# Kernel tuning notes

Measured on AMD Instinct MI355X. Metric: run time of the kernel, lower is better.

## Reference

```python
import jax, jax.numpy as jnp
import numpy as np

N, D = 65536, 1024  # points, in_dim == out_dim (required by the module's double use of linear.weight)


def setup_inputs() -> dict:
    key = jax.random.key(0)
    k_x, k_w, k_W, k_noise = jax.random.split(key, 4)
    x = jax.random.normal(k_x, (N, D), dtype=jnp.float32)
    w = jax.random.normal(k_w, (D,), dtype=jnp.float32)  # style vector (len == in_dim)
    # learned params of nn.Linear(in_dim, out_dim)
    W = jax.random.normal(k_W, (D, D), dtype=jnp.float32) * 0.02  # [out_dim, in_dim]
    b = jnp.zeros((D,), dtype=jnp.float32)
    # noise path: torch does randn(1, out_dim) * noise_strength each forward;
    # we materialize the raw noise deterministically for reproducibility.
    noise_strength = jnp.full((1,), 0.1, dtype=jnp.float32)
    noise_raw = jax.random.normal(k_noise, (1, D), dtype=jnp.float32)
    return {"x": x, "w": w, "W": W, "b": b,
            "noise_strength": noise_strength, "noise_raw": noise_raw}


def reference(x, w, W, b, noise_strength, noise_raw):
    # 1) plain linear: x1 = x @ W.T + b            [N, D]
    x1 = x @ W.T + b
    # 2) modulated_linear(x1, W, styles=w, noise, demodulate=True)
    #    demod coefficients: rsqrt(sum_j (W[o,j]*w[j])^2 + 1e-8)   [D]
    dcoefs = jax.lax.rsqrt(jnp.sum(jnp.square(W * w[None, :]), axis=1) + 1e-8)
    #    modulate input, dense matmul with raw weight
    x2 = (x1 * w) @ W.T                            # [N, D]
    #    fma: x2 * dcoefs + noise
    noise = noise_raw * noise_strength             # [1, D]
    x3 = x2 * dcoefs[None, :] + noise
    # 3) bias add + leaky_relu (torch default negative_slope=0.01)
    return jax.nn.leaky_relu(x3 + b, negative_slope=0.01)
```

## Files before the change

kernel.cpp:

```cpp
#include <hip/hip_runtime.h>
#include <hip/hip_bf16.h>

using bf16 = __hip_bfloat16;
typedef __attribute__((ext_vector_type(8))) short bf16x8;
typedef __attribute__((ext_vector_type(4))) float f32x4;

#define DDIM 1024

__device__ __forceinline__ void gload16(const bf16* g, bf16* l) {
    __builtin_amdgcn_global_load_lds(
        (const __attribute__((address_space(1))) void*)g,
        (__attribute__((address_space(3))) void*)l, 16, 0, 0);
}
__device__ __forceinline__ short f2b(float f) {
    return (short)__bfloat16_as_ushort(__float2bfloat16(f));
}


__global__ void prep_kernel(const float* __restrict__ W, const float* __restrict__ w,
                            const float* __restrict__ b, const float* __restrict__ nstr,
                            const float* __restrict__ nraw,
                            float* __restrict__ dco, float* __restrict__ add,
                            bf16* __restrict__ Qb) {
    int o = blockIdx.x;
    int lane = threadIdx.x;
    const float* Wrow = W + (size_t)o * DDIM;
    bf16* Qrow = Qb + (size_t)o * DDIM;
    float s = 0.f, c = 0.f;
    for (int j = lane; j < DDIM; j += 64) {
        float wv = Wrow[j], sv = w[j];
        float q = wv * sv;
        Qrow[j] = __float2bfloat16(q);
        s += q * q;
        c += b[j] * q;
    }
#pragma unroll
    for (int off = 32; off; off >>= 1) {
        s += __shfl_down(s, off);
        c += __shfl_down(c, off);
    }
    if (lane == 0) {
        float d = rsqrtf(s + 1e-8f);
        dco[o] = d;
        add[o] = c * d + nraw[o] * nstr[0] + b[o];
    }
}

__global__ void transpose_kernel(const float* __restrict__ W, bf16* __restrict__ Wt) {
    __shared__ bf16 tile[64][72];
    int bi = blockIdx.x * 64;
    int bj = blockIdx.y * 64;
    int r  = threadIdx.x >> 2;
    int c4 = (threadIdx.x & 3) * 16;
    const float* src = W + (size_t)(bi + r) * DDIM + bj + c4;
#pragma unroll
    for (int i = 0; i < 16; ++i) tile[r][c4 + i] = __float2bfloat16(src[i]);
    __syncthreads();
    bf16* dst = Wt + (size_t)(bj + r) * DDIM + bi + c4;
#pragma unroll
    for (int i = 0; i < 16; ++i) dst[i] = tile[c4 + i][r];
}

__global__ __launch_bounds__(256) void mgemm(const bf16* __restrict__ A,
                                             const bf16* __restrict__ B,
                                             bf16* __restrict__ C) {
    __shared__ bf16 lA[128 * 32];
    __shared__ bf16 lB[128 * 32];
    int tid  = threadIdx.x;
    int lane = tid & 63, wid = tid >> 6;
    int wr = wid >> 1, wc = wid & 1;
    int brow = blockIdx.x >> 3;
    int bcol = blockIdx.x & 7;

    const bf16* Ab = A + (size_t)brow * 128 * DDIM;
    const bf16* Bb = B + (size_t)bcol * 128 * DDIM;
    int srow = tid >> 2;
    int scol = (tid & 3) * 8;

    f32x4 acc[4][4];
#pragma unroll
    for (int m = 0; m < 4; ++m)
#pragma unroll
        for (int n = 0; n < 4; ++n) acc[m][n] = (f32x4){0.f, 0.f, 0.f, 0.f};

    int r16 = lane & 15, kh = lane >> 4;

    for (int k0 = 0; k0 < DDIM; k0 += 32) {
        gload16(Ab + (size_t)srow * DDIM + k0 + scol,        lA + tid * 8);
        gload16(Ab + (size_t)(srow + 64) * DDIM + k0 + scol, lA + (tid + 256) * 8);
        gload16(Bb + (size_t)srow * DDIM + k0 + scol,        lB + tid * 8);
        gload16(Bb + (size_t)(srow + 64) * DDIM + k0 + scol, lB + (tid + 256) * 8);
        __syncthreads();
        bf16x8 aF[4], bF[4];
#pragma unroll
        for (int m = 0; m < 4; ++m) {
            aF[m] = *(const bf16x8*)(lA + ((wr * 64 + m * 16 + r16) * 32 + kh * 8));
            bF[m] = *(const bf16x8*)(lB + ((wc * 64 + m * 16 + r16) * 32 + kh * 8));
        }
#pragma unroll
        for (int m = 0; m < 4; ++m)
#pragma unroll
            for (int n = 0; n < 4; ++n)
                acc[m][n] = __builtin_amdgcn_mfma_f32_16x16x32_bf16(aF[m], bF[n], acc[m][n], 0, 0, 0);
        __syncthreads();
    }

    int cb = lane & 15;
    int rb = (lane >> 4) * 4;
#pragma unroll
    for (int n = 0; n < 4; ++n) {
        int col = bcol * 128 + wc * 64 + n * 16 + cb;
#pragma unroll
        for (int m = 0; m < 4; ++m)
#pragma unroll
            for (int j = 0; j < 4; ++j) {
                int row = wr * 64 + m * 16 + rb + j;
                C[((size_t)brow * 128 + row) * DDIM + col] = __float2bfloat16(acc[m][n][j]);
            }
    }
}

#define BAR()  __builtin_amdgcn_s_barrier()
#define VMW(n) asm volatile("s_waitcnt vmcnt(" #n ")")
#define LGW()  asm volatile("s_waitcnt lgkmcnt(0)")

__global__ __launch_bounds__(512, 2) void big_gemm(
    const float* __restrict__ Af, const bf16* __restrict__ Bw,
    const float* __restrict__ dco, const float* __restrict__ add,
    float* __restrict__ Cf)
{
    __shared__ bf16 sA[2][2][256 * 32];
    __shared__ bf16 sB[2][2][256 * 32];

    const int tid  = threadIdx.x;
    const int lane = tid & 63;
    const int wid  = tid >> 6;
    const int wr   = wid >> 2, wc = wid & 3;
    const int r16  = lane & 15, kh = lane >> 4;
    const int fso  = (kh ^ ((r16 >> 1) & 3)) * 8;

    int bx  = blockIdx.x;
    int swz = (bx & 7) * 128 + (bx >> 3);
    int brow = swz >> 2, bcol = swz & 3;

    const float* Asrc_f = Af + (size_t)(brow * 256) * DDIM;
    const bf16*  Bsrc   = Bw + (size_t)(bcol * 256) * DDIM;

    const int sr  = tid >> 2;
    const int ssl = (tid & 3) ^ ((sr >> 1) & 3);

    f32x4 acc[8][4];
#pragma unroll
    for (int m = 0; m < 8; ++m)
#pragma unroll
        for (int n = 0; n < 4; ++n) acc[m][n] = (f32x4){0.f, 0.f, 0.f, 0.f};

    bf16x8 aF[4], bF[4];
    float4 gA0, gA1, gA2, gA3;
    float4 gB0, gB1, gB2, gB3;

#define STAGE_B(buf, kt, ks) do { \
    const bf16* _s = Bsrc + (size_t)sr * DDIM + ((kt) * 64 + (ks) * 32 + ssl * 8); \
    gload16(_s,               &sB[buf][ks][tid * 8]); \
    gload16(_s + 128 * DDIM,  &sB[buf][ks][(tid + 512) * 8]); \
} while (0)

#define LOAD_A_F(g0, g1, g2, g3, kt, ks) do { \
    const float* _p = Asrc_f + (size_t)sr * DDIM + ((kt) * 64 + (ks) * 32 + (tid & 3) * 8); \
    g0 = ((const float4*)_p)[0]; g1 = ((const float4*)_p)[1]; \
    const float* _q = _p + 128 * DDIM; \
    g2 = ((const float4*)_q)[0]; g3 = ((const float4*)_q)[1]; \
} while (0)

#define WRITE_A(buf, ks, g0, g1, g2, g3) do { \
    bf16x8 _pk; \
    _pk[0]=f2b(g0.x); _pk[1]=f2b(g0.y); _pk[2]=f2b(g0.z); _pk[3]=f2b(g0.w); \
    _pk[4]=f2b(g1.x); _pk[5]=f2b(g1.y); _pk[6]=f2b(g1.z); _pk[7]=f2b(g1.w); \
    *(bf16x8*)&sA[buf][ks][sr * 32 + ssl * 8] = _pk; \
    _pk[0]=f2b(g2.x); _pk[1]=f2b(g2.y); _pk[2]=f2b(g2.z); _pk[3]=f2b(g2.w); \
    _pk[4]=f2b(g3.x); _pk[5]=f2b(g3.y); _pk[6]=f2b(g3.z); _pk[7]=f2b(g3.w); \
    *(bf16x8*)&sA[buf][ks][(sr + 128) * 32 + ssl * 8] = _pk; \
} while (0)

#define RD_A(buf, ks, mh) do { \
    _Pragma("unroll") for (int _m = 0; _m < 4; ++_m) \
        aF[_m] = *(const bf16x8*)&sA[buf][ks][(wr * 128 + (mh) * 64 + _m * 16 + r16) * 32 + fso]; \
} while (0)

#define RD_B(buf, ks) do { \
    _Pragma("unroll") for (int _n = 0; _n < 4; ++_n) \
        bF[_n] = *(const bf16x8*)&sB[buf][ks][(wc * 64 + _n * 16 + r16) * 32 + fso]; \
} while (0)

#define MFMA16(mh) do { \
    __builtin_amdgcn_s_setprio(1); \
    _Pragma("unroll") for (int _m = 0; _m < 4; ++_m) { \
        acc[(mh)*4+_m][0] = __builtin_amdgcn_mfma_f32_16x16x32_bf16(aF[_m], bF[0], acc[(mh)*4+_m][0], 0, 0, 0); \
        acc[(mh)*4+_m][1] = __builtin_amdgcn_mfma_f32_16x16x32_bf16(aF[_m], bF[1], acc[(mh)*4+_m][1], 0, 0, 0); \
        acc[(mh)*4+_m][2] = __builtin_amdgcn_mfma_f32_16x16x32_bf16(aF[_m], bF[2], acc[(mh)*4+_m][2], 0, 0, 0); \
        acc[(mh)*4+_m][3] = __builtin_amdgcn_mfma_f32_16x16x32_bf16(aF[_m], bF[3], acc[(mh)*4+_m][3], 0, 0, 0); \
    } \
    __builtin_amdgcn_s_setprio(0); \
} while (0)

    LOAD_A_F(gA0, gA1, gA2, gA3, 0, 0);
    LOAD_A_F(gB0, gB1, gB2, gB3, 0, 1);
    STAGE_B(0, 0, 0); STAGE_B(0, 0, 1);
    WRITE_A(0, 0, gA0, gA1, gA2, gA3);
    WRITE_A(0, 1, gB0, gB1, gB2, gB3);
    LOAD_A_F(gA0, gA1, gA2, gA3, 1, 0);
    LOAD_A_F(gB0, gB1, gB2, gB3, 1, 1);
    LGW();
    VMW(8);
    BAR();

    for (int i = 0; i < 8; ++i) {
        int t2 = 2 * i + 2; if (t2 > 15) t2 = 15;
        int t3 = 2 * i + 3; if (t3 > 15) t3 = 15;
        int t1 = 2 * i + 1;

        RD_A(0, 0, 0); RD_B(0, 0);
        WRITE_A(1, 0, gA0, gA1, gA2, gA3);
        LOAD_A_F(gA0, gA1, gA2, gA3, t2, 0);
        LGW();
        BAR(); MFMA16(0); BAR();
        RD_A(0, 0, 1);
        STAGE_B(1, t1, 0);
        BAR(); MFMA16(1); VMW(6); BAR();
        RD_A(0, 1, 0); RD_B(0, 1);
        WRITE_A(1, 1, gB0, gB1, gB2, gB3);
        LOAD_A_F(gB0, gB1, gB2, gB3, t2, 1);
        LGW();
        BAR(); MFMA16(0); BAR();
        RD_A(0, 1, 1);
        STAGE_B(1, t1, 1);
        BAR(); MFMA16(1); VMW(6); BAR();
        RD_A(1, 0, 0); RD_B(1, 0);
        WRITE_A(0, 0, gA0, gA1, gA2, gA3);
        LOAD_A_F(gA0, gA1, gA2, gA3, t3, 0);
        LGW();
        BAR(); MFMA16(0); BAR();
        RD_A(1, 0, 1);
        STAGE_B(0, t2, 0);
        BAR(); MFMA16(1); VMW(6); BAR();
        RD_A(1, 1, 0); RD_B(1, 1);
        WRITE_A(0, 1, gB0, gB1, gB2, gB3);
        LOAD_A_F(gB0, gB1, gB2, gB3, t3, 1);
        LGW();
        BAR(); MFMA16(0); BAR();
        RD_A(1, 1, 1);
        STAGE_B(0, t2, 1);
        BAR(); MFMA16(1); VMW(6); BAR();
    }

    int crb = brow * 256 + wr * 128 + kh * 4;
    int ccb = bcol * 256 + wc * 64 + r16;
#pragma unroll
    for (int n = 0; n < 4; ++n) {
        int col = ccb + n * 16;
        float cm = dco[col], ca = add[col];
#pragma unroll
        for (int m = 0; m < 8; ++m) {
#pragma unroll
            for (int j = 0; j < 4; ++j) {
                size_t idx = (size_t)(crb + m * 16 + j) * DDIM + col;
                float v = acc[m][n][j] * cm + ca;
                v = (v >= 0.f) ? v : 0.01f * v;
                Cf[idx] = v;
            }
        }
    }
#undef STAGE_B
#undef LOAD_A_F
#undef WRITE_A
#undef RD_A
#undef RD_B
#undef MFMA16
}

extern "C" void kernel_launch(void* const* d_in, const int* in_sizes, int n_in,
                              void* d_out, int out_size, void* d_ws, size_t ws_size,
                              hipStream_t stream) {
    const float* x  = (const float*)d_in[0];
    const float* w  = (const float*)d_in[1];
    const float* W  = (const float*)d_in[2];
    const float* b  = (const float*)d_in[3];
    const float* ns = (const float*)d_in[4];
    const float* nr = (const float*)d_in[5];
    float* out = (float*)d_out;

    float* dco = (float*)d_ws;
    float* add = dco + DDIM;
    bf16*  Qb  = (bf16*)((char*)d_ws + 8192);
    bf16*  Wt  = (bf16*)((char*)d_ws + 8192 + 2097152);
    bf16*  Mt  = (bf16*)((char*)d_ws + 8192 + 2 * 2097152);

    int M = in_sizes[0] / DDIM;
    int grid = (M / 256) * (DDIM / 256);

    prep_kernel<<<DDIM, 64, 0, stream>>>(W, w, b, ns, nr, dco, add, Qb);
    transpose_kernel<<<dim3(16, 16), 256, 0, stream>>>(W, Wt);
    mgemm<<<64, 256, 0, stream>>>(Qb, Wt, Mt);
    big_gemm<<<grid, 512, 0, stream>>>(x, Mt, dco, add, out);
}
```

Before: 295.1 us.

## Shrink big GEMM tile to 256x128 with a single-stage K=32 pipeline

Reworks the main fused GEMM from 256x256 output tiles with a two-half K=64 software pipeline into 256x128 tiles. It now uses a simpler K=32 double-buffered loop, half the accumulators, smaller LDS buffers, a launch bound asking for 4 blocks per CU, and twice as many blocks. The aim is more resident waves and fewer barriers per MFMA phase to hide latency. In exchange, the fp32 activation matrix is re-read for twice as many column tiles, and each tile does less compute per byte loaded. The prep kernel edit is cosmetic.

```diff
diff --git a/kernel.cpp b/kernel.cpp
--- a/kernel.cpp
+++ b/kernel.cpp
@@ -28,8 +28,7 @@
     bf16* Qrow = Qb + (size_t)o * DDIM;
     float s = 0.f, c = 0.f;
     for (int j = lane; j < DDIM; j += 64) {
-        float wv = Wrow[j], sv = w[j];
-        float q = wv * sv;
+        float q = Wrow[j] * w[j];
         Qrow[j] = __float2bfloat16(q);
         s += q * q;
         c += b[j] * q;
@@ -71,20 +70,16 @@
     int wr = wid >> 1, wc = wid & 1;
     int brow = blockIdx.x >> 3;
     int bcol = blockIdx.x & 7;
-
     const bf16* Ab = A + (size_t)brow * 128 * DDIM;
     const bf16* Bb = B + (size_t)bcol * 128 * DDIM;
     int srow = tid >> 2;
     int scol = (tid & 3) * 8;
-
     f32x4 acc[4][4];
 #pragma unroll
     for (int m = 0; m < 4; ++m)
 #pragma unroll
         for (int n = 0; n < 4; ++n) acc[m][n] = (f32x4){0.f, 0.f, 0.f, 0.f};
-
     int r16 = lane & 15, kh = lane >> 4;
-
     for (int k0 = 0; k0 < DDIM; k0 += 32) {
         gload16(Ab + (size_t)srow * DDIM + k0 + scol,        lA + tid * 8);
         gload16(Ab + (size_t)(srow + 64) * DDIM + k0 + scol, lA + (tid + 256) * 8);
@@ -104,7 +99,6 @@
                 acc[m][n] = __builtin_amdgcn_mfma_f32_16x16x32_bf16(aF[m], bF[n], acc[m][n], 0, 0, 0);
         __syncthreads();
     }
-
     int cb = lane & 15;
     int rb = (lane >> 4) * 4;
 #pragma unroll
@@ -124,149 +118,123 @@
 #define VMW(n) asm volatile("s_waitcnt vmcnt(" #n ")")
 #define LGW()  asm volatile("s_waitcnt lgkmcnt(0)")
 
-__global__ __launch_bounds__(512, 2) void big_gemm(
+__global__ __launch_bounds__(512, 4) void big_gemm(
     const float* __restrict__ Af, const bf16* __restrict__ Bw,
     const float* __restrict__ dco, const float* __restrict__ add,
     float* __restrict__ Cf)
 {
-    __shared__ bf16 sA[2][2][256 * 32];
-    __shared__ bf16 sB[2][2][256 * 32];
+    __shared__ bf16 sA[2][256 * 32];
+    __shared__ bf16 sB[2][128 * 32];
 
     const int tid  = threadIdx.x;
     const int lane = tid & 63;
     const int wid  = tid >> 6;
-    const int wr   = wid >> 2, wc = wid & 3;
+    const int wr   = wid >> 1, wc = wid & 1;
     const int r16  = lane & 15, kh = lane >> 4;
     const int fso  = (kh ^ ((r16 >> 1) & 3)) * 8;
 
     int bx  = blockIdx.x;
-    int swz = (bx & 7) * 128 + (bx >> 3);
-    int brow = swz >> 2, bcol = swz & 3;
+    int swz = (bx & 7) * 256 + (bx >> 3);
+    int brow = swz >> 3, bcol = swz & 7;
 
     const float* Asrc_f = Af + (size_t)(brow * 256) * DDIM;
-    const bf16*  Bsrc   = Bw + (size_t)(bcol * 256) * DDIM;
+    const bf16*  Bsrc   = Bw + (size_t)(bcol * 128) * DDIM;
 
     const int sr  = tid >> 2;
     const int ssl = (tid & 3) ^ ((sr >> 1) & 3);
 
-    f32x4 acc[8][4];
-#pragma unroll
-    for (int m = 0; m < 8; ++m)
+    f32x4 acc[4][4];
+#pragma unroll
+    for (int m = 0; m < 4; ++m)
 #pragma unroll
         for (int n = 0; n < 4; ++n) acc[m][n] = (f32x4){0.f, 0.f, 0.f, 0.f};
 
     bf16x8 aF[4], bF[4];
     float4 gA0, gA1, gA2, gA3;
-    float4 gB0, gB1, gB2, gB3;
-
-#define STAGE_B(buf, kt, ks) do { \
-    const bf16* _s = Bsrc + (size_t)sr * DDIM + ((kt) * 64 + (ks) * 32 + ssl * 8); \
-    gload16(_s,               &sB[buf][ks][tid * 8]); \
-    gload16(_s + 128 * DDIM,  &sB[buf][ks][(tid + 512) * 8]); \
-} while (0)
-
-#define LOAD_A_F(g0, g1, g2, g3, kt, ks) do { \
-    const float* _p = Asrc_f + (size_t)sr * DDIM + ((kt) * 64 + (ks) * 32 + (tid & 3) * 8); \
-    g0 = ((const float4*)_p)[0]; g1 = ((const float4*)_p)[1]; \
+
+#define STAGE_B(buf, kt) do { \
+    const bf16* _s = Bsrc + (size_t)sr * DDIM + ((kt) * 32 + ssl * 8); \
+    gload16(_s, &sB[buf][tid * 8]); \
+} while (0)
+
+#define LOAD_A_F(kt) do { \
+    const float* _p = Asrc_f + (size_t)sr * DDIM + ((kt) * 32 + (tid & 3) * 8); \
+    gA0 = ((const float4*)_p)[0]; gA1 = ((const float4*)_p)[1]; \
     const float* _q = _p + 128 * DDIM; \
-    g2 = ((const float4*)_q)[0]; g3 = ((const float4*)_q)[1]; \
-} while (0)
-
-#define WRITE_A(buf, ks, g0, g1, g2, g3) do { \
+    gA2 = ((const float4*)_q)[0]; gA3 = ((const float4*)_q)[1]; \
+} while (0)
+
+#define WRITE_A(buf) do { \
     bf16x8 _pk; \
-    _pk[0]=f2b(g0.x); _pk[1]=f2b(g0.y); _pk[2]=f2b(g0.z); _pk[3]=f2b(g0.w); \
-    _pk[4]=f2b(g1.x); _pk[5]=f2b(g1.y); _pk[6]=f2b(g1.z); _pk[7]=f2b(g1.w); \
-    *(bf16x8*)&sA[buf][ks][sr * 32 + ssl * 8] = _pk; \
-    _pk[0]=f2b(g2.x); _pk[1]=f2b(g2.y); _pk[2]=f2b(g2.z); _pk[3]=f2b(g2.w); \
-    _pk[4]=f2b(g3.x); _pk[5]=f2b(g3.y); _pk[6]=f2b(g3.z); _pk[7]=f2b(g3.w); \
-    *(bf16x8*)&sA[buf][ks][(sr + 128) * 32 + ssl * 8] = _pk; \
-} while (0)
-
-#define RD_A(buf, ks, mh) do { \
+    _pk[0]=f2b(gA0.x); _pk[1]=f2b(gA0.y); _pk[2]=f2b(gA0.z); _pk[3]=f2b(gA0.w); \
+    _pk[4]=f2b(gA1.x); _pk[5]=f2b(gA1.y); _pk[6]=f2b(gA1.z); _pk[7]=f2b(gA1.w); \
+    *(bf16x8*)&sA[buf][sr * 32 + ssl * 8] = _pk; \
+    _pk[0]=f2b(gA2.x); _pk[1]=f2b(gA2.y); _pk[2]=f2b(gA2.z); _pk[3]=f2b(gA2.w); \
+    _pk[4]=f2b(gA3.x); _pk[5]=f2b(gA3.y); _pk[6]=f2b(gA3.z); _pk[7]=f2b(gA3.w); \
+    *(bf16x8*)&sA[buf][(sr + 128) * 32 + ssl * 8] = _pk; \
+} while (0)
+
+#define RD_A(buf) do { \
     _Pragma("unroll") for (int _m = 0; _m < 4; ++_m) \
-        aF[_m] = *(const bf16x8*)&sA[buf][ks][(wr * 128 + (mh) * 64 + _m * 16 + r16) * 32 + fso]; \
-} while (0)
-
-#define RD_B(buf, ks) do { \
+        aF[_m] = *(const bf16x8*)&sA[buf][(wr * 64 + _m * 16 + r16) * 32 + fso]; \
+} while (0)
+
+#define RD_B(buf) do { \
     _Pragma("unroll") for (int _n = 0; _n < 4; ++_n) \
-        bF[_n] = *(const bf16x8*)&sB[buf][ks][(wc * 64 + _n * 16 + r16) * 32 + fso]; \
-} while (0)
-
-#define MFMA16(mh) do { \
+        bF[_n] = *(const bf16x8*)&sB[buf][(wc * 64 + _n * 16 + r16) * 32 + fso]; \
+} while (0)
+
+#define MFMA16() do { \
     __builtin_amdgcn_s_setprio(1); \
     _Pragma("unroll") for (int _m = 0; _m < 4; ++_m) { \
-        acc[(mh)*4+_m][0] = __builtin_amdgcn_mfma_f32_16x16x32_bf16(aF[_m], bF[0], acc[(mh)*4+_m][0], 0, 0, 0); \
-        acc[(mh)*4+_m][1] = __builtin_amdgcn_mfma_f32_16x16x32_bf16(aF[_m], bF[1], acc[(mh)*4+_m][1], 0, 0, 0); \
-        acc[(mh)*4+_m][2] = __builtin_amdgcn_mfma_f32_16x16x32_bf16(aF[_m], bF[2], acc[(mh)*4+_m][2], 0, 0, 0); \
-        acc[(mh)*4+_m][3] = __builtin_amdgcn_mfma_f32_16x16x32_bf16(aF[_m], bF[3], acc[(mh)*4+_m][3], 0, 0, 0); \
+        acc[_m][0] = __builtin_amdgcn_mfma_f32_16x16x32_bf16(aF[_m], bF[0], acc[_m][0], 0, 0, 0); \
+        acc[_m][1] = __builtin_amdgcn_mfma_f32_16x16x32_bf16(aF[_m], bF[1], acc[_m][1], 0, 0, 0); \
+        acc[_m][2] = __builtin_amdgcn_mfma_f32_16x16x32_bf16(aF[_m], bF[2], acc[_m][2], 0, 0, 0); \
+        acc[_m][3] = __builtin_amdgcn_mfma_f32_16x16x32_bf16(aF[_m], bF[3], acc[_m][3], 0, 0, 0); \
     } \
     __builtin_amdgcn_s_setprio(0); \
 } while (0)
 
-    LOAD_A_F(gA0, gA1, gA2, gA3, 0, 0);
-    LOAD_A_F(gB0, gB1, gB2, gB3, 0, 1);
-    STAGE_B(0, 0, 0); STAGE_B(0, 0, 1);
-    WRITE_A(0, 0, gA0, gA1, gA2, gA3);
-    WRITE_A(0, 1, gB0, gB1, gB2, gB3);
-    LOAD_A_F(gA0, gA1, gA2, gA3, 1, 0);
-    LOAD_A_F(gB0, gB1, gB2, gB3, 1, 1);
+    LOAD_A_F(0);
+    STAGE_B(0, 0);
+    VMW(1);
+    WRITE_A(0);
+    LOAD_A_F(1);
     LGW();
-    VMW(8);
+    VMW(4);
     BAR();
 
-    for (int i = 0; i < 8; ++i) {
-        int t2 = 2 * i + 2; if (t2 > 15) t2 = 15;
-        int t3 = 2 * i + 3; if (t3 > 15) t3 = 15;
-        int t1 = 2 * i + 1;
-
-        RD_A(0, 0, 0); RD_B(0, 0);
-        WRITE_A(1, 0, gA0, gA1, gA2, gA3);
-        LOAD_A_F(gA0, gA1, gA2, gA3, t2, 0);
+    for (int t = 0; t < 32; ++t) {
+        int cur = t & 1, nxt = cur ^ 1;
+        int t1 = t + 1; if (t1 > 31) t1 = 31;
+        int t2 = t + 2; if (t2 > 31) t2 = 31;
+
+        RD_A(cur); RD_B(cur);
+        STAGE_B(nxt, t1);
+        VMW(1);
+        WRITE_A(nxt);
+        LOAD_A_F(t2);
         LGW();
-        BAR(); MFMA16(0); BAR();
-        RD_A(0, 0, 1);
-        STAGE_B(1, t1, 0);
-        BAR(); MFMA16(1); VMW(6); BAR();
-        RD_A(0, 1, 0); RD_B(0, 1);
-        WRITE_A(1, 1, gB0, gB1, gB2, gB3);
-        LOAD_A_F(gB0, gB1, gB2, gB3, t2, 1);
-        LGW();
-        BAR(); MFMA16(0); BAR();
-        RD_A(0, 1, 1);
-        STAGE_B(1, t1, 1);
-        BAR(); MFMA16(1); VMW(6); BAR();
-        RD_A(1, 0, 0); RD_B(1, 0);
-        WRITE_A(0, 0, gA0, gA1, gA2, gA3);
-        LOAD_A_F(gA0, gA1, gA2, gA3, t3, 0);
-        LGW();
-        BAR(); MFMA16(0); BAR();
-        RD_A(1, 0, 1);
-        STAGE_B(0, t2, 0);
-        BAR(); MFMA16(1); VMW(6); BAR();
-        RD_A(1, 1, 0); RD_B(1, 1);
-        WRITE_A(0, 1, gB0, gB1, gB2, gB3);
-        LOAD_A_F(gB0, gB1, gB2, gB3, t3, 1);
-        LGW();
-        BAR(); MFMA16(0); BAR();
-        RD_A(1, 1, 1);
-        STAGE_B(0, t2, 1);
-        BAR(); MFMA16(1); VMW(6); BAR();
-    }
-
-    int crb = brow * 256 + wr * 128 + kh * 4;
-    int ccb = bcol * 256 + wc * 64 + r16;
+        BAR();
+        MFMA16();
+        VMW(4);
+        BAR();
+    }
+
+    int cb = lane & 15;
+    int rb = (lane >> 4) * 4;
 #pragma unroll
     for (int n = 0; n < 4; ++n) {
-        int col = ccb + n * 16;
+        int col = bcol * 128 + wc * 64 + n * 16 + cb;
         float cm = dco[col], ca = add[col];
 #pragma unroll
-        for (int m = 0; m < 8; ++m) {
+        for (int m = 0; m < 4; ++m) {
 #pragma unroll
             for (int j = 0; j < 4; ++j) {
-                size_t idx = (size_t)(crb + m * 16 + j) * DDIM + col;
+                int row = brow * 256 + wr * 64 + m * 16 + rb + j;
                 float v = acc[m][n][j] * cm + ca;
                 v = (v >= 0.f) ? v : 0.01f * v;
-                Cf[idx] = v;
+                Cf[(size_t)row * DDIM + col] = v;
             }
         }
     }
@@ -296,7 +264,7 @@
     bf16*  Mt  = (bf16*)((char*)d_ws + 8192 + 2 * 2097152);
 
     int M = in_sizes[0] / DDIM;
-    int grid = (M / 256) * (DDIM / 256);
+    int grid = (M / 256) * (DDIM / 128);
 
     prep_kernel<<<DDIM, 64, 0, stream>>>(W, w, b, ns, nr, dco, add, Qb);
     transpose_kernel<<<dim3(16, 16), 256, 0, stream>>>(W, Wt);
```

Result: no change. 298.1 us (+1.0%).

## Restructure main GEMM pipeline to 32-MFMA phases with fewer barriers

Applied to the files above, without the earlier changes.

Rewrites the main fused GEMM's k-loop so each phase loads both A halves into two fragment register sets and issues 32 MFMAs between barriers, instead of 16 MFMAs per half-step. The goal is fewer barriers and LDS-read stalls per k-tile. B staging for the next tile is now issued together, and the vmcnt waits are rearranged. This raises register pressure from the extra fragment array, and the changed wait counts could mis-order global loads against LDS writes.

```diff
diff --git a/kernel.cpp b/kernel.cpp
--- a/kernel.cpp
+++ b/kernel.cpp
@@ -28,8 +28,7 @@
     bf16* Qrow = Qb + (size_t)o * DDIM;
     float s = 0.f, c = 0.f;
     for (int j = lane; j < DDIM; j += 64) {
-        float wv = Wrow[j], sv = w[j];
-        float q = wv * sv;
+        float q = Wrow[j] * w[j];
         Qrow[j] = __float2bfloat16(q);
         s += q * q;
         c += b[j] * q;
@@ -71,20 +70,16 @@
     int wr = wid >> 1, wc = wid & 1;
     int brow = blockIdx.x >> 3;
     int bcol = blockIdx.x & 7;
-
     const bf16* Ab = A + (size_t)brow * 128 * DDIM;
     const bf16* Bb = B + (size_t)bcol * 128 * DDIM;
     int srow = tid >> 2;
     int scol = (tid & 3) * 8;
-
     f32x4 acc[4][4];
 #pragma unroll
     for (int m = 0; m < 4; ++m)
 #pragma unroll
         for (int n = 0; n < 4; ++n) acc[m][n] = (f32x4){0.f, 0.f, 0.f, 0.f};
-
     int r16 = lane & 15, kh = lane >> 4;
-
     for (int k0 = 0; k0 < DDIM; k0 += 32) {
         gload16(Ab + (size_t)srow * DDIM + k0 + scol,        lA + tid * 8);
         gload16(Ab + (size_t)(srow + 64) * DDIM + k0 + scol, lA + (tid + 256) * 8);
@@ -104,7 +99,6 @@
                 acc[m][n] = __builtin_amdgcn_mfma_f32_16x16x32_bf16(aF[m], bF[n], acc[m][n], 0, 0, 0);
         __syncthreads();
     }
-
     int cb = lane & 15;
     int rb = (lane >> 4) * 4;
 #pragma unroll
@@ -155,7 +149,7 @@
 #pragma unroll
         for (int n = 0; n < 4; ++n) acc[m][n] = (f32x4){0.f, 0.f, 0.f, 0.f};
 
-    bf16x8 aF[4], bF[4];
+    bf16x8 aF[4], aF2[4], bF[4];
     float4 gA0, gA1, gA2, gA3;
     float4 gB0, gB1, gB2, gB3;
 
@@ -182,9 +176,9 @@
     *(bf16x8*)&sA[buf][ks][(sr + 128) * 32 + ssl * 8] = _pk; \
 } while (0)
 
-#define RD_A(buf, ks, mh) do { \
+#define RD_A(dst, buf, ks, mh) do { \
     _Pragma("unroll") for (int _m = 0; _m < 4; ++_m) \
-        aF[_m] = *(const bf16x8*)&sA[buf][ks][(wr * 128 + (mh) * 64 + _m * 16 + r16) * 32 + fso]; \
+        dst[_m] = *(const bf16x8*)&sA[buf][ks][(wr * 128 + (mh) * 64 + _m * 16 + r16) * 32 + fso]; \
 } while (0)
 
 #define RD_B(buf, ks) do { \
@@ -192,21 +186,30 @@
         bF[_n] = *(const bf16x8*)&sB[buf][ks][(wc * 64 + _n * 16 + r16) * 32 + fso]; \
 } while (0)
 
-#define MFMA16(mh) do { \
+#define MFMA32() do { \
     __builtin_amdgcn_s_setprio(1); \
     _Pragma("unroll") for (int _m = 0; _m < 4; ++_m) { \
-        acc[(mh)*4+_m][0] = __builtin_amdgcn_mfma_f32_16x16x32_bf16(aF[_m], bF[0], acc[(mh)*4+_m][0], 0, 0, 0); \
-        acc[(mh)*4+_m][1] = __builtin_amdgcn_mfma_f32_16x16x32_bf16(aF[_m], bF[1], acc[(mh)*4+_m][1], 0, 0, 0); \
-        acc[(mh)*4+_m][2] = __builtin_amdgcn_mfma_f32_16x16x32_bf16(aF[_m], bF[2], acc[(mh)*4+_m][2], 0, 0, 0); \
-        acc[(mh)*4+_m][3] = __builtin_amdgcn_mfma_f32_16x16x32_bf16(aF[_m], bF[3], acc[(mh)*4+_m][3], 0, 0, 0); \
+        acc[_m][0] = __builtin_amdgcn_mfma_f32_16x16x32_bf16(aF[_m], bF[0], acc[_m][0], 0, 0, 0); \
+        acc[_m][1] = __builtin_amdgcn_mfma_f32_16x16x32_bf16(aF[_m], bF[1], acc[_m][1], 0, 0, 0); \
+        acc[_m][2] = __builtin_amdgcn_mfma_f32_16x16x32_bf16(aF[_m], bF[2], acc[_m][2], 0, 0, 0); \
+        acc[_m][3] = __builtin_amdgcn_mfma_f32_16x16x32_bf16(aF[_m], bF[3], acc[_m][3], 0, 0, 0); \
+    } \
+    _Pragma("unroll") for (int _m = 0; _m < 4; ++_m) { \
+        acc[4+_m][0] = __builtin_amdgcn_mfma_f32_16x16x32_bf16(aF2[_m], bF[0], acc[4+_m][0], 0, 0, 0); \
+        acc[4+_m][1] = __builtin_amdgcn_mfma_f32_16x16x32_bf16(aF2[_m], bF[1], acc[4+_m][1], 0, 0, 0); \
+        acc[4+_m][2] = __builtin_amdgcn_mfma_f32_16x16x32_bf16(aF2[_m], bF[2], acc[4+_m][2], 0, 0, 0); \
+        acc[4+_m][3] = __builtin_amdgcn_mfma_f32_16x16x32_bf16(aF2[_m], bF[3], acc[4+_m][3], 0, 0, 0); \
     } \
     __builtin_amdgcn_s_setprio(0); \
 } while (0)
 
     LOAD_A_F(gA0, gA1, gA2, gA3, 0, 0);
     LOAD_A_F(gB0, gB1, gB2, gB3, 0, 1);
-    STAGE_B(0, 0, 0); STAGE_B(0, 0, 1);
+    STAGE_B(0, 0, 0);
+    STAGE_B(0, 0, 1);
+    VMW(8);
     WRITE_A(0, 0, gA0, gA1, gA2, gA3);
+    VMW(4);
     WRITE_A(0, 1, gB0, gB1, gB2, gB3);
     LOAD_A_F(gA0, gA1, gA2, gA3, 1, 0);
     LOAD_A_F(gB0, gB1, gB2, gB3, 1, 1);
@@ -214,43 +217,35 @@
     VMW(8);
     BAR();
 
-    for (int i = 0; i < 8; ++i) {
-        int t2 = 2 * i + 2; if (t2 > 15) t2 = 15;
-        int t3 = 2 * i + 3; if (t3 > 15) t3 = 15;
-        int t1 = 2 * i + 1;
-
-        RD_A(0, 0, 0); RD_B(0, 0);
-        WRITE_A(1, 0, gA0, gA1, gA2, gA3);
+    for (int t = 0; t < 16; ++t) {
+        int b = t & 1, nb = b ^ 1;
+        int t1 = t + 1; if (t1 > 15) t1 = 15;
+        int t2 = t + 2; if (t2 > 15) t2 = 15;
+
+        RD_A(aF,  b, 0, 0);
+        RD_A(aF2, b, 0, 1);
+        RD_B(b, 0);
+        VMW(4);
+        WRITE_A(nb, 0, gA0, gA1, gA2, gA3);
+        STAGE_B(nb, t1, 0);
+        STAGE_B(nb, t1, 1);
+        LGW();
+        BAR();
+        MFMA32();
+        BAR();
+
+        RD_A(aF,  b, 1, 0);
+        RD_A(aF2, b, 1, 1);
+        RD_B(b, 1);
+        VMW(4);
+        WRITE_A(nb, 1, gB0, gB1, gB2, gB3);
         LOAD_A_F(gA0, gA1, gA2, gA3, t2, 0);
-        LGW();
-        BAR(); MFMA16(0); BAR();
-        RD_A(0, 0, 1);
-        STAGE_B(1, t1, 0);
-        BAR(); MFMA16(1); VMW(6); BAR();
-        RD_A(0, 1, 0); RD_B(0, 1);
-        WRITE_A(1, 1, gB0, gB1, gB2, gB3);
         LOAD_A_F(gB0, gB1, gB2, gB3, t2, 1);
         LGW();
-        BAR(); MFMA16(0); BAR();
-        RD_A(0, 1, 1);
-        STAGE_B(1, t1, 1);
-        BAR(); MFMA16(1); VMW(6); BAR();
-        RD_A(1, 0, 0); RD_B(1, 0);
-        WRITE_A(0, 0, gA0, gA1, gA2, gA3);
-        LOAD_A_F(gA0, gA1, gA2, gA3, t3, 0);
-        LGW();
-        BAR(); MFMA16(0); BAR();
-        RD_A(1, 0, 1);
-        STAGE_B(0, t2, 0);
-        BAR(); MFMA16(1); VMW(6); BAR();
-        RD_A(1, 1, 0); RD_B(1, 1);
-        WRITE_A(0, 1, gB0, gB1, gB2, gB3);
-        LOAD_A_F(gB0, gB1, gB2, gB3, t3, 1);
-        LGW();
-        BAR(); MFMA16(0); BAR();
-        RD_A(1, 1, 1);
-        STAGE_B(0, t2, 1);
-        BAR(); MFMA16(1); VMW(6); BAR();
+        BAR();
+        MFMA32();
+        VMW(8);
+        BAR();
     }
 
     int crb = brow * 256 + wr * 128 + kh * 4;
@@ -275,7 +270,7 @@
 #undef WRITE_A
 #undef RD_A
 #undef RD_B
-#undef MFMA16
+#undef MFMA32
 }
 
 extern "C" void kernel_launch(void* const* d_in, const int* in_sizes, int n_in,
```

Measured after the change: 273.3 us. -7.4%, faster.
